# Kernel optimization log

Hardware: AMD Instinct MI355X
Metric: run time of the kernel (lower is better)

Reference implementation:

```python
import jax, jax.numpy as jnp
import numpy as np

N = 100000   # nodes
E = 3200000  # edges
G = 512      # graphs in batch
EPS = 1e-5   # batchnorm eps


def _lin(key, fan_in, fan_out):
    return jax.random.normal(key, (fan_in, fan_out), jnp.float32) / np.sqrt(fan_in)


def setup_inputs() -> dict:
    key = jax.random.key(0)
    ks = jax.random.split(key, 12)
    x = jax.random.normal(ks[0], (N, 2), jnp.float32)
    edge_index = jax.random.randint(ks[1], (2, E), 0, N, dtype=jnp.int64)
    batch_index = jnp.sort(jax.random.randint(ks[2], (N,), 0, G, dtype=jnp.int64))
    w = (8, 32, 128)
    return {
        "x": x, "edge_index": edge_index, "batch_index": batch_index,
        "W1": _lin(ks[3], 2, w[0]),   "b1": jnp.zeros((w[0],), jnp.float32),
        "g1": jnp.ones((w[0],), jnp.float32),  "be1": jnp.zeros((w[0],), jnp.float32),
        "W2": _lin(ks[4], w[0], w[1]), "b2": jnp.zeros((w[1],), jnp.float32),
        "g2": jnp.ones((w[1],), jnp.float32),  "be2": jnp.zeros((w[1],), jnp.float32),
        "W3": _lin(ks[5], w[1], w[2]), "b3": jnp.zeros((w[2],), jnp.float32),
        "g3": jnp.ones((w[2],), jnp.float32),  "be3": jnp.zeros((w[2],), jnp.float32),
        "Wl": _lin(ks[6], w[2], 3),    "bl": jnp.zeros((3,), jnp.float32),
    }


def _gcn_norm(edge_index):
    # add self loops, symmetric normalization (PyG GCNConv default)
    loops = jnp.arange(N, dtype=edge_index.dtype)
    src = jnp.concatenate([edge_index[0], loops])
    dst = jnp.concatenate([edge_index[1], loops])
    deg = jax.ops.segment_sum(jnp.ones_like(dst, jnp.float32), dst, num_segments=N)
    dis = jnp.where(deg > 0, jax.lax.rsqrt(jnp.maximum(deg, 1.0)), 0.0)
    norm = dis[src] * dis[dst]  # [E+N]
    return src, dst, norm


def _gcn_conv(h, W, b, src, dst, norm):
    h = h @ W                                   # [N, out]
    msg = h[src] * norm[:, None]                # gather + scale
    return jax.ops.segment_sum(msg, dst, num_segments=N) + b


def _bn(h, g, b):
    # training-mode batchnorm over node dim
    m = jnp.mean(h, axis=0)
    v = jnp.mean(jnp.square(h - m), axis=0)
    return (h - m) * jax.lax.rsqrt(v + EPS) * g + b


def reference(x, edge_index, batch_index, W1, b1, g1, be1, W2, b2, g2, be2,
              W3, b3, g3, be3, Wl, bl):
    src, dst, norm = _gcn_norm(edge_index)
    h = _bn(jax.nn.relu(_gcn_conv(x, W1, b1, src, dst, norm)), g1, be1)
    h = _bn(jax.nn.relu(_gcn_conv(h, W2, b2, src, dst, norm)), g2, be2)
    h = _bn(jax.nn.relu(_gcn_conv(h, W3, b3, src, dst, norm)), g3, be3)
    pooled = jax.ops.segment_max(h, batch_index, num_segments=G)  # [G, 128]
    logits = pooled @ Wl + bl                                     # [G, 3]
    return jax.nn.log_softmax(logits, axis=1)
```

## Files before the change

### kernel.cpp

```cpp
#include <hip/hip_runtime.h>
#include <hip/hip_bf16.h>
#include <hip/hip_fp16.h>
#include <math.h>

#define N_NODES 100000
#define N_EDGES 3200000
#define N_GRAPHS 512
#define BN_EPS 1e-5f
#define NBIN ((N_NODES + 511) / 512)
#define CHUNK 8192
#define NCHUNK ((N_EDGES + CHUNK - 1) / CHUNK)
#define STORE_CAP (N_EDGES + 16 * NBIN * NCHUNK)
#define NMMB ((N_NODES + 63) / 64)
#define NB2 3125
#define NB2P 3136
#define PLANE2 ((size_t)(N_NODES + 1) * 16)
#define PLANEU ((size_t)N_NODES * 16)
#define A1CAP 1024
#define A2CAP 2048
#define A3CAP 2048

typedef _Float16 half8_t __attribute__((ext_vector_type(8)));
typedef float float4_t __attribute__((ext_vector_type(4)));

struct alignas(8) h4 { __half2 a, b; };
struct alignas(16) h8s { __half2 h[4]; };



__global__ void k_hist2(const int* __restrict__ dst, int* __restrict__ hists) {
    __shared__ int h[NBIN];
    for (int i = threadIdx.x; i < NBIN; i += blockDim.x) h[i] = 0;
    __syncthreads();
    int e0 = blockIdx.x * CHUNK;
    int e1 = min(e0 + CHUNK, N_EDGES);
    int e = e0 + threadIdx.x * 8;
    if (e + 8 <= e1) {
        int4 d0 = *(const int4*)(dst + e);
        int4 d1 = *(const int4*)(dst + e + 4);
        atomicAdd(&h[d0.x >> 9], 1); atomicAdd(&h[d0.y >> 9], 1);
        atomicAdd(&h[d0.z >> 9], 1); atomicAdd(&h[d0.w >> 9], 1);
        atomicAdd(&h[d1.x >> 9], 1); atomicAdd(&h[d1.y >> 9], 1);
        atomicAdd(&h[d1.z >> 9], 1); atomicAdd(&h[d1.w >> 9], 1);
    } else {
        for (; e < e1; ++e) atomicAdd(&h[dst[e] >> 9], 1);
    }
    __syncthreads();
    for (int i = threadIdx.x; i < NBIN; i += blockDim.x)
        hists[i * NCHUNK + blockIdx.x] = h[i];
}

__global__ void k_scan2(int* __restrict__ hists, int* __restrict__ ghist) {
    int b = blockIdx.x;
    int lane = threadIdx.x;
    int carry = 0;
    int base = b * NCHUNK;
    for (int c0 = 0; c0 < NCHUNK; c0 += 64) {
        int c = c0 + lane;
        int v = (c < NCHUNK) ? hists[base + c] : 0;
        int pv = (v + 15) & ~15;
        int inc = pv;
#pragma unroll
        for (int off = 1; off < 64; off <<= 1) {
            int u = __shfl_up(inc, off, 64);
            if (lane >= off) inc += u;
        }
        if (c < NCHUNK) hists[base + c] = inc - pv + carry;
        carry += __shfl(inc, 63, 64);
    }
    if (lane == 0) ghist[b] = carry;
}

__global__ void k_binscan(const int* __restrict__ ghist, int* __restrict__ bbase) {
    __shared__ int sd[512];
    int t = threadIdx.x;
    int v = (t < NBIN) ? ghist[t] : 0;
    sd[t] = v;
    __syncthreads();
    for (int off = 1; off < 512; off <<= 1) {
        int u = (t >= off) ? sd[t - off] : 0;
        __syncthreads();
        sd[t] += u;
        __syncthreads();
    }
    if (t < NBIN) bbase[t] = sd[t] - v;
    if (t == 511) bbase[NBIN] = sd[511];
}

__global__ void k_scatter(const int* __restrict__ src, const int* __restrict__ dst,
                          const int* __restrict__ bbase, const int* __restrict__ hists,
                          int* __restrict__ store) {
    __shared__ int cur[NBIN];
    for (int i = threadIdx.x; i < NBIN; i += blockDim.x)
        cur[i] = bbase[i] + hists[i * NCHUNK + blockIdx.x];
    __syncthreads();
    int e0 = blockIdx.x * CHUNK;
    int e1 = min(e0 + CHUNK, N_EDGES);
    int e = e0 + threadIdx.x * 8;
    if (e + 8 <= e1) {
        int4 d0 = *(const int4*)(dst + e), d1 = *(const int4*)(dst + e + 4);
        int4 s0 = *(const int4*)(src + e), s1 = *(const int4*)(src + e + 4);
        int dd[8] = {d0.x, d0.y, d0.z, d0.w, d1.x, d1.y, d1.z, d1.w};
        int sv[8] = {s0.x, s0.y, s0.z, s0.w, s1.x, s1.y, s1.z, s1.w};
#pragma unroll
        for (int j = 0; j < 8; ++j) {
            int d = dd[j];
            int b = d >> 9;
            int pos = atomicAdd(&cur[b], 1);
            store[pos] = (sv[j] << 9) | (d & 511);
        }
    } else {
        for (; e < e1; ++e) {
            int d = dst[e];
            int b = d >> 9;
            int pos = atomicAdd(&cur[b], 1);
            store[pos] = (src[e] << 9) | (d & 511);
        }
    }
    __syncthreads();
    for (int i = threadIdx.x; i < NBIN; i += blockDim.x) {
        int p = cur[i];
        int end = (p + 15) & ~15;
        for (; p < end; ++p) store[p] = -1;
    }
}

__global__ void k_csr_build(const int* __restrict__ bbase, const int* __restrict__ store,
                            const float* __restrict__ x, int* __restrict__ offs,
                            int* __restrict__ ends, float* __restrict__ dis,
                            float* __restrict__ rdis, float4* __restrict__ xd,
                            int* __restrict__ csr) {
    __shared__ int cnt[512], cur[512], wsum[4];
    int b = blockIdx.x;
    int n0 = b << 9;
    int e0 = bbase[b], e1 = bbase[b + 1];
    int t = threadIdx.x;
    int lane = t & 63, wid = t >> 6;
    if (t < 512) cnt[t] = 0;
    __syncthreads();
    for (int e = e0 + t; e < e1; e += 4096) {
        int p[4];
#pragma unroll
        for (int j = 0; j < 4; ++j)
            p[j] = (e + 1024 * j < e1) ? store[e + 1024 * j] : -1;
#pragma unroll
        for (int j = 0; j < 4; ++j)
            if (p[j] >= 0) atomicAdd(&cnt[p[j] & 511], 1);
    }
    __syncthreads();
    int c0 = 0, c1 = 0, pair = 0, inc = 0;
    if (t < 256) {
        c0 = cnt[2 * t];
        c1 = cnt[2 * t + 1];
        pair = c0 + c1;
        inc = pair;
#pragma unroll
        for (int off = 1; off < 64; off <<= 1) {
            int u = __shfl_up(inc, off, 64);
            if (lane >= off) inc += u;
        }
        if (lane == 63) wsum[wid] = inc;
    }
    __syncthreads();
    if (t < 256) {
        int wo = 0;
        for (int w = 0; w < wid; ++w) wo += wsum[w];
        int ex = inc - pair + wo;
        cur[2 * t] = ex;
        cur[2 * t + 1] = ex + c0;
#pragma unroll
        for (int j = 0; j < 2; ++j) {
            int n = n0 + 2 * t + j;
            int cc = j ? c1 : c0;
            int exx = j ? ex + c0 : ex;
            if (n < N_NODES) {
                offs[n] = e0 + exx;
                ends[n] = e0 + exx + cc;
                float dn = rsqrtf(1.0f + (float)cc);
                dis[n] = dn;
                rdis[n] = sqrtf(1.0f + (float)cc);
                float2 xv = *(const float2*)(x + 2 * (size_t)n);
                xd[n] = make_float4(dn * xv.x, dn * xv.y, dn, 0.f);
            } else if (n == N_NODES) {
                xd[N_NODES] = make_float4(0.f, 0.f, 0.f, 0.f);
            }
        }
    }
    __syncthreads();
    for (int e = e0 + t; e < e1; e += 4096) {
        int p[4];
#pragma unroll
        for (int j = 0; j < 4; ++j)
            p[j] = (e + 1024 * j < e1) ? store[e + 1024 * j] : -1;
#pragma unroll
        for (int j = 0; j < 4; ++j)
            if (p[j] >= 0) {
                int pos = e0 + atomicAdd(&cur[p[j] & 511], 1);
                csr[pos] = p[j] >> 9;
            }
    }
}


__global__ void k_agg1(const float4* __restrict__ xd, const int* __restrict__ offs,
                       const int* __restrict__ ends, const int* __restrict__ csr,
                       const float* __restrict__ W1, const float* __restrict__ b1,
                       float* __restrict__ svec, __half* __restrict__ ys1) {
    __shared__ float sW[16], sb[8];
    __shared__ int sidx[A1CAP], soff[16], send[16];
    int t = threadIdx.x;
    int n0 = blockIdx.x * 16;
    if (t < 16) { sW[t] = W1[t]; soff[t] = offs[n0 + t]; send[t] = ends[n0 + t]; }
    if (t >= 16 && t < 24) sb[t - 16] = b1[t - 16];
    __syncthreads();
    int base = soff[0];
    int span = send[15] - base;
    int cap = min(span, A1CAP);
    for (int i = t; i < cap; i += 256) sidx[i] = csr[base + i];
    __syncthreads();

    int nl = t >> 4;
    int lane16 = t & 15;
    int node = n0 + nl;
    int rb = soff[nl] - base;
    int re = send[nl] - base;
    float ax = 0.f, ay = 0.f, as = 0.f;
    for (int r = rb + lane16; r < re; r += 64) {
        int s[4];
#pragma unroll
        for (int j = 0; j < 4; ++j) {
            int rr = r + 16 * j;
            s[j] = (rr < re) ? ((rr < A1CAP) ? sidx[rr] : csr[base + rr]) : N_NODES;
        }
        float4 v[4];
#pragma unroll
        for (int j = 0; j < 4; ++j) v[j] = xd[s[j]];
#pragma unroll
        for (int j = 0; j < 4; ++j) {
            ax += v[j].x;
            ay += v[j].y;
            as += v[j].z;
        }
    }
#pragma unroll
    for (int off = 1; off < 16; off <<= 1) {
        ax += __shfl_xor(ax, off, 64);
        ay += __shfl_xor(ay, off, 64);
        as += __shfl_xor(as, off, 64);
    }
    if (lane16 == 0) {
        float4 xn = xd[node];
        float dn = xn.z;
        float u0x = dn * (ax + xn.x);
        float u0y = dn * (ay + xn.y);
        svec[node] = dn * (as + xn.z);
        float y[8];
#pragma unroll
        for (int f = 0; f < 8; ++f)
            y[f] = dn * fmaxf(u0x * sW[f] + u0y * sW[8 + f] + sb[f], 0.f);
        h8s o;
#pragma unroll
        for (int q = 0; q < 4; ++q) o.h[q] = __floats2half2_rn(y[2 * q], y[2 * q + 1]);
        *(h8s*)(ys1 + (size_t)node * 8) = o;
    }
}


__global__ void k_stats8v(const __half* __restrict__ ys1, const float* __restrict__ rdis,
                          float* __restrict__ stats) {
    int t = threadIdx.x;
    float s[8] = {0, 0, 0, 0, 0, 0, 0, 0};
    float s2[8] = {0, 0, 0, 0, 0, 0, 0, 0};
    for (int n = blockIdx.x * 256 + t; n < N_NODES; n += gridDim.x * 256) {
        float r = rdis[n];
        h8s v = *(const h8s*)(ys1 + (size_t)n * 8);
#pragma unroll
        for (int q = 0; q < 4; ++q) {
            float v0 = __low2float(v.h[q]) * r;
            float v1 = __high2float(v.h[q]) * r;
            s[2 * q] += v0;      s2[2 * q] += v0 * v0;
            s[2 * q + 1] += v1;  s2[2 * q + 1] += v1 * v1;
        }
    }
#pragma unroll
    for (int off = 1; off < 64; off <<= 1)
#pragma unroll
        for (int k = 0; k < 8; ++k) {
            s[k] += __shfl_xor(s[k], off, 64);
            s2[k] += __shfl_xor(s2[k], off, 64);
        }
    __shared__ float sm[16];
    if (t < 16) sm[t] = 0.f;
    __syncthreads();
    if ((t & 63) == 0) {
#pragma unroll
        for (int k = 0; k < 8; ++k) {
            atomicAdd(&sm[k], s[k]);
            atomicAdd(&sm[8 + k], s2[k]);
        }
    }
    __syncthreads();
    if (t < 16) atomicAdd(&stats[t], sm[t]);
}


__global__ void k_prep2(const float* __restrict__ stats, const float* __restrict__ gamma,
                        const float* __restrict__ beta, const float* __restrict__ W2,
                        float* __restrict__ W2p, float* __restrict__ cw2,
                        __half* __restrict__ ys1) {
    __shared__ float a1[8], c1[8];
    int t = threadIdx.x;
    if (t < 8) {
        float inv_n = 1.0f / (float)N_NODES;
        float m = stats[t] * inv_n;
        float v = stats[8 + t] * inv_n - m * m;
        float a = gamma[t] * rsqrtf(v + BN_EPS);
        a1[t] = a;
        c1[t] = beta[t] - m * a;
    }
    __syncthreads();
    W2p[t] = a1[t >> 5] * W2[t];
    if (t < 32) {
        float cb = 0.f;
#pragma unroll
        for (int i = 0; i < 8; ++i) cb += c1[i] * W2[i * 32 + t];
        cw2[t] = cb;
    }
    if (t == 128) *(int4*)(ys1 + (size_t)N_NODES * 8) = make_int4(0, 0, 0, 0);
}


__global__ void k_agg2(const __half* __restrict__ ys1, const int* __restrict__ offs,
                       const int* __restrict__ ends, const int* __restrict__ csr,
                       const float* __restrict__ dis, const float* __restrict__ svec,
                       const float* __restrict__ W2p, const float* __restrict__ cw2,
                       const float* __restrict__ b2, __half* __restrict__ ys2,
                       float* __restrict__ part2) {
    __shared__ float sW[256], sC[32], sB[32], sm2[64];
    __shared__ int sidx[A2CAP], soff[32], send[32];
    int t = threadIdx.x;
    int n0 = blockIdx.x * 32;
    sW[t] = W2p[t];
    if (t < 32) {
        sC[t] = cw2[t]; sB[t] = b2[t];
        soff[t] = offs[n0 + t]; send[t] = ends[n0 + t];
    }
    if (t < 64) sm2[t] = 0.f;
    __syncthreads();
    int base = soff[0];
    int span = send[31] - base;
    int cap = min(span, A2CAP);
    for (int i = t; i < cap; i += 256) sidx[i] = csr[base + i];
    __syncthreads();

    int nl = t >> 3;
    int lane8 = t & 7;
    int node = n0 + nl;
    int rb = soff[nl] - base;
    int re = send[nl] - base;
    float a[8] = {0, 0, 0, 0, 0, 0, 0, 0};
    int r = rb + lane8;
    if (span <= A2CAP) {
        for (; r + 24 < re; r += 32) {
            int s0 = sidx[r], s1 = sidx[r + 8], s2i = sidx[r + 16], s3 = sidx[r + 24];
            h8s v0 = *(const h8s*)(ys1 + (size_t)s0 * 8);
            h8s v1 = *(const h8s*)(ys1 + (size_t)s1 * 8);
            h8s v2 = *(const h8s*)(ys1 + (size_t)s2i * 8);
            h8s v3 = *(const h8s*)(ys1 + (size_t)s3 * 8);
#pragma unroll
            for (int q = 0; q < 4; ++q) {
                a[2 * q] += __low2float(v0.h[q]) + __low2float(v1.h[q]) +
                            __low2float(v2.h[q]) + __low2float(v3.h[q]);
                a[2 * q + 1] += __high2float(v0.h[q]) + __high2float(v1.h[q]) +
                                __high2float(v2.h[q]) + __high2float(v3.h[q]);
            }
        }
        if (r < re) {
            int s[4];
#pragma unroll
            for (int j = 0; j < 4; ++j) {
                int rr = r + 8 * j;
                s[j] = (rr < re) ? sidx[rr] : N_NODES;
            }
            h8s v[4];
#pragma unroll
            for (int j = 0; j < 4; ++j) v[j] = *(const h8s*)(ys1 + (size_t)s[j] * 8);
#pragma unroll
            for (int j = 0; j < 4; ++j)
#pragma unroll
                for (int q = 0; q < 4; ++q) {
                    a[2 * q] += __low2float(v[j].h[q]);
                    a[2 * q + 1] += __high2float(v[j].h[q]);
                }
        }
    } else {
        for (; r < re; r += 32) {
            int s[4];
#pragma unroll
            for (int j = 0; j < 4; ++j) {
                int rr = r + 8 * j;
                s[j] = (rr < re) ? ((rr < A2CAP) ? sidx[rr] : csr[base + rr]) : N_NODES;
            }
            h8s v[4];
#pragma unroll
            for (int j = 0; j < 4; ++j) v[j] = *(const h8s*)(ys1 + (size_t)s[j] * 8);
#pragma unroll
            for (int j = 0; j < 4; ++j)
#pragma unroll
                for (int q = 0; q < 4; ++q) {
                    a[2 * q] += __low2float(v[j].h[q]);
                    a[2 * q + 1] += __high2float(v[j].h[q]);
                }
        }
    }
    if (lane8 == 0) {
        h8s v = *(const h8s*)(ys1 + (size_t)node * 8);
#pragma unroll
        for (int q = 0; q < 4; ++q) {
            a[2 * q] += __low2float(v.h[q]);
            a[2 * q + 1] += __high2float(v.h[q]);
        }
    }
#pragma unroll
    for (int off = 1; off < 8; off <<= 1)
#pragma unroll
        for (int k = 0; k < 8; ++k) a[k] += __shfl_xor(a[k], off, 64);
    int lane = t & 63;
    int nsub = lane >> 3;
    int lb = nsub << 3;
    float u[8];
#pragma unroll
    for (int i = 0; i < 8; ++i) u[i] = __shfl(a[i], lb, 64);
    float dn = dis[node];
    float sv = svec[node];
#pragma unroll
    for (int i = 0; i < 8; ++i) u[i] *= dn;
    int c0 = (lane & 7) * 4;
    float hh[4], hs2[4];
#pragma unroll
    for (int k = 0; k < 4; ++k) {
        int col = c0 + k;
        float conv = sB[col] + sv * sC[col];
#pragma unroll
        for (int i = 0; i < 8; ++i) conv += u[i] * sW[i * 32 + col];
        hh[k] = fmaxf(conv, 0.f);
        hs2[k] = hh[k] * hh[k];
    }
    h4 o;
    o.a = __floats2half2_rn(dn * hh[0], dn * hh[1]);
    o.b = __floats2half2_rn(dn * hh[2], dn * hh[3]);
    *(h4*)(ys2 + (size_t)(c0 >> 4) * PLANE2 + (size_t)node * 16 + (c0 & 15)) = o;

    float hs[4];
#pragma unroll
    for (int k = 0; k < 4; ++k) hs[k] = hh[k];
#pragma unroll
    for (int off = 8; off < 64; off <<= 1)
#pragma unroll
        for (int k = 0; k < 4; ++k) {
            hs[k] += __shfl_xor(hs[k], off, 64);
            hs2[k] += __shfl_xor(hs2[k], off, 64);
        }
    if (nsub == 0) {
#pragma unroll
        for (int k = 0; k < 4; ++k) {
            atomicAdd(&sm2[c0 + k], hs[k]);
            atomicAdd(&sm2[32 + c0 + k], hs2[k]);
        }
    }
    __syncthreads();
    if (t < 64) part2[(size_t)t * NB2P + blockIdx.x] = sm2[t];
}

__global__ void k_red32(const float* __restrict__ part2, float* __restrict__ stats2) {
    int i = blockIdx.x;
    int t = threadIdx.x;
    float s = 0.f;
    for (int b = t; b < NB2; b += 256) s += part2[(size_t)i * NB2P + b];
    __shared__ float sm[256];
    sm[t] = s;
    __syncthreads();
    for (int st = 128; st > 0; st >>= 1) {
        if (t < st) sm[t] += sm[t + st];
        __syncthreads();
    }
    if (t == 0) stats2[i] = sm[0];
}


__global__ void k_prep3(const float* __restrict__ stats, const float* __restrict__ gamma,
                        const float* __restrict__ beta, const float* __restrict__ W3,
                        __half* __restrict__ wfrag, float* __restrict__ cw3,
                        __half* __restrict__ ys2) {
    __shared__ float a2[32], c2[32];
    int t = threadIdx.x;
    if (t < 32) {
        float inv_n = 1.0f / (float)N_NODES;
        float m = stats[t] * inv_n;
        float v = stats[32 + t] * inv_n - m * m;
        float a = gamma[t] * rsqrtf(v + BN_EPS);
        a2[t] = a;
        c2[t] = beta[t] - m * a;
    }
    __syncthreads();
    {
        int g = t >> 6, kq = (t >> 4) & 3, c = t & 15;
#pragma unroll
        for (int j = 0; j < 8; ++j) {
            int k = kq * 8 + j;
            wfrag[(size_t)t * 8 + j] = __float2half(a2[k] * W3[k * 128 + g * 16 + c]);
        }
    }
    if (t < 128) {
        float cb = 0.f;
#pragma unroll
        for (int k = 0; k < 32; ++k) cb += c2[k] * W3[k * 128 + t];
        cw3[t] = cb;
    }
    if (t >= 480 && t < 496) {
        int idx = t - 480;
        ((__half2*)(ys2 + (size_t)(idx >> 3) * PLANE2 + (size_t)N_NODES * 16))[idx & 7] =
            __half2{__float2half(0.f), __float2half(0.f)};
    }
}


__global__ void k_agg3(const __half* __restrict__ ys2, const int* __restrict__ offs,
                       const int* __restrict__ ends, const int* __restrict__ csr,
                       const float* __restrict__ dis, __half* __restrict__ u2) {
    __shared__ int sidx[A3CAP], soff[32], send[32];
    int plane = blockIdx.x & 1;
    int nb = blockIdx.x >> 1;
    int t = threadIdx.x;
    int n0 = nb * 32;
    if (t < 32) { soff[t] = offs[n0 + t]; send[t] = ends[n0 + t]; }
    __syncthreads();
    int base = soff[0];
    int span = send[31] - base;
    int cap = min(span, A3CAP);
    for (int i = t; i < cap; i += 512) sidx[i] = csr[base + i];
    __syncthreads();

    int nl = t >> 4;
    int lane16 = t & 15;
    int eg = lane16 >> 1;
    int chunk = lane16 & 1;
    int node = n0 + nl;
    int rb = soff[nl] - base;
    int re = send[nl] - base;
    float a[8] = {0, 0, 0, 0, 0, 0, 0, 0};
    const __half* hp = ys2 + (size_t)plane * PLANE2 + chunk * 8;
    int r = rb + eg;
    if (span <= A3CAP) {
        for (; r + 24 < re; r += 32) {
            int s0 = sidx[r], s1 = sidx[r + 8], s2i = sidx[r + 16], s3 = sidx[r + 24];
            h8s v0 = *(const h8s*)(hp + (size_t)s0 * 16);
            h8s v1 = *(const h8s*)(hp + (size_t)s1 * 16);
            h8s v2 = *(const h8s*)(hp + (size_t)s2i * 16);
            h8s v3 = *(const h8s*)(hp + (size_t)s3 * 16);
#pragma unroll
            for (int q = 0; q < 4; ++q) {
                a[2 * q] += __low2float(v0.h[q]) + __low2float(v1.h[q]) +
                            __low2float(v2.h[q]) + __low2float(v3.h[q]);
                a[2 * q + 1] += __high2float(v0.h[q]) + __high2float(v1.h[q]) +
                                __high2float(v2.h[q]) + __high2float(v3.h[q]);
            }
        }
        if (r < re) {
            int s[4];
#pragma unroll
            for (int j = 0; j < 4; ++j) {
                int rr = r + 8 * j;
                s[j] = (rr < re) ? sidx[rr] : N_NODES;
            }
            h8s v[4];
#pragma unroll
            for (int j = 0; j < 4; ++j) v[j] = *(const h8s*)(hp + (size_t)s[j] * 16);
#pragma unroll
            for (int j = 0; j < 4; ++j)
#pragma unroll
                for (int q = 0; q < 4; ++q) {
                    a[2 * q] += __low2float(v[j].h[q]);
                    a[2 * q + 1] += __high2float(v[j].h[q]);
                }
        }
    } else {
        for (; r < re; r += 32) {
            int s[4];
#pragma unroll
            for (int j = 0; j < 4; ++j) {
                int rr = r + 8 * j;
                s[j] = (rr < re) ? ((rr < A3CAP) ? sidx[rr] : csr[base + rr]) : N_NODES;
            }
            h8s v[4];
#pragma unroll
            for (int j = 0; j < 4; ++j) v[j] = *(const h8s*)(hp + (size_t)s[j] * 16);
#pragma unroll
            for (int j = 0; j < 4; ++j)
#pragma unroll
                for (int q = 0; q < 4; ++q) {
                    a[2 * q] += __low2float(v[j].h[q]);
                    a[2 * q + 1] += __high2float(v[j].h[q]);
                }
        }
    }
    if (eg == 0) {
        h8s v = *(const h8s*)(hp + (size_t)node * 16);
#pragma unroll
        for (int q = 0; q < 4; ++q) {
            a[2 * q] += __low2float(v.h[q]);
            a[2 * q + 1] += __high2float(v.h[q]);
        }
    }
#pragma unroll
    for (int off = 2; off < 16; off <<= 1)
#pragma unroll
        for (int k = 0; k < 8; ++k) a[k] += __shfl_xor(a[k], off, 64);
    if (eg == 0) {
        float dn = dis[node];
        h8s o;
#pragma unroll
        for (int q = 0; q < 4; ++q)
            o.h[q] = __floats2half2_rn(dn * a[2 * q], dn * a[2 * q + 1]);
        *(h8s*)(u2 + (size_t)plane * PLANEU + (size_t)node * 16 + chunk * 8) = o;
    }
}


__global__ void k_mm_mfma(const __half* __restrict__ u2, const __half* __restrict__ wfrag,
                          const float* __restrict__ cw3, const float* __restrict__ b3,
                          const float* __restrict__ svec, const int* __restrict__ batch,
                          float* __restrict__ spart, int* __restrict__ gmax,
                          int* __restrict__ gmin) {
    __shared__ float sm[256];
    int t = threadIdx.x;
    int wave = t >> 6;
    int lane = t & 63;
    int n0 = (blockIdx.x * 4 + wave) * 16;
    bool active = n0 < N_NODES;
    int m = lane & 15;
    int kq = lane >> 4;
    float ss[8] = {0, 0, 0, 0, 0, 0, 0, 0};
    float ss2[8] = {0, 0, 0, 0, 0, 0, 0, 0};

    if (active) {
        half8_t af = *(const half8_t*)(u2 + (size_t)(kq >> 1) * PLANEU +
                                       (size_t)(n0 + m) * 16 + (kq & 1) * 8);
        float4_t accs[8];
#pragma unroll
        for (int g = 0; g < 8; ++g) {
            float4_t acc = {0.f, 0.f, 0.f, 0.f};
            half8_t bf = *(const half8_t*)(wfrag + (size_t)((g * 4 + kq) * 16 + m) * 8);
            accs[g] = __builtin_amdgcn_mfma_f32_16x16x32_f16(af, bf, acc, 0, 0, 0);
        }
        float sv[4];
#pragma unroll
        for (int r = 0; r < 4; ++r) sv[r] = svec[n0 + kq * 4 + r];

        int b_first = batch[n0];
        int b_last = batch[n0 + 15];
        bool uni = (b_first == b_last);
        int bnr[4];
        if (!uni) {
#pragma unroll
            for (int r = 0; r < 4; ++r) bnr[r] = batch[n0 + kq * 4 + r];
        }
        float ymx[8], ymn[8];
#pragma unroll
        for (int g = 0; g < 8; ++g) {
            float cwf = cw3[g * 16 + m];
            float bf3 = b3[g * 16 + m];
            float mx = 0.f, mn = INFINITY;
#pragma unroll
            for (int r = 0; r < 4; ++r) {
                float y = fmaxf(accs[g][r] + sv[r] * cwf + bf3, 0.f);
                ss[g] += y;
                ss2[g] += y * y;
                mx = fmaxf(mx, y);
                mn = fminf(mn, y);
                if (!uni) {
                    int yb = __float_as_int(y);
                    atomicMax(&gmax[bnr[r] * 128 + g * 16 + m], yb);
                    atomicMin(&gmin[bnr[r] * 128 + g * 16 + m], yb);
                }
            }
            ymx[g] = mx;
            ymn[g] = mn;
        }
        if (uni) {
#pragma unroll
            for (int off = 16; off < 64; off <<= 1)
#pragma unroll
                for (int g = 0; g < 8; ++g) {
                    ymx[g] = fmaxf(ymx[g], __shfl_xor(ymx[g], off, 64));
                    ymn[g] = fminf(ymn[g], __shfl_xor(ymn[g], off, 64));
                }
            if (kq == 0) {
#pragma unroll
                for (int g = 0; g < 8; ++g) {
                    atomicMax(&gmax[b_first * 128 + g * 16 + m], __float_as_int(ymx[g]));
                    atomicMin(&gmin[b_first * 128 + g * 16 + m], __float_as_int(ymn[g]));
                }
            }
        }
    }
#pragma unroll
    for (int off = 16; off < 64; off <<= 1)
#pragma unroll
        for (int g = 0; g < 8; ++g) {
            ss[g] += __shfl_xor(ss[g], off, 64);
            ss2[g] += __shfl_xor(ss2[g], off, 64);
        }
    sm[t] = 0.f;
    __syncthreads();
    if (active && kq == 0) {
#pragma unroll
        for (int g = 0; g < 8; ++g) {
            atomicAdd(&sm[g * 16 + m], ss[g]);
            atomicAdd(&sm[128 + g * 16 + m], ss2[g]);
        }
    }
    __syncthreads();
    spart[(size_t)blockIdx.x * 256 + t] = sm[t];
}

__global__ void k_stats_red(const float* __restrict__ part, float* __restrict__ stats) {
    int i = blockIdx.x;
    int t = threadIdx.x;
    float s = 0.f;
    for (int b = t; b < NMMB; b += 256) s += part[(size_t)b * 256 + i];
    __shared__ float sm[256];
    sm[t] = s;
    __syncthreads();
    for (int st = 128; st > 0; st >>= 1) {
        if (t < st) sm[t] += sm[t + st];
        __syncthreads();
    }
    if (t == 0) stats[i] = sm[0];
}


__device__ __forceinline__ int lower_bound_dev(const int* __restrict__ a, int val) {
    int lo = 0, hi = N_NODES;
    while (lo < hi) {
        int mid = (lo + hi) >> 1;
        if (a[mid] < val) lo = mid + 1; else hi = mid;
    }
    return lo;
}

__global__ void k_poolhead(const int* __restrict__ gmax, const int* __restrict__ gmin,
                           const int* __restrict__ batch, const float* __restrict__ stats,
                           const float* __restrict__ gamma, const float* __restrict__ beta,
                           const float* __restrict__ Wl, const float* __restrict__ bl,
                           float* __restrict__ out) {
    int g = blockIdx.x;
    int f = threadIdx.x;
    float inv_n = 1.0f / (float)N_NODES;
    float m = stats[f] * inv_n;
    float var = stats[128 + f] * inv_n - m * m;
    float a = gamma[f] * rsqrtf(var + BN_EPS);
    float c = beta[f] - m * a;
    int s = lower_bound_dev(batch, g);
    int e = lower_bound_dev(batch, g + 1);
    float mx = __int_as_float(gmax[g * 128 + f]);
    float mn = __int_as_float(gmin[g * 128 + f]);
    float r;
    if (e > s) r = (a >= 0.f) ? (a * mx + c) : (a * mn + c);
    else r = -INFINITY;
    __shared__ float l[3][128];
    l[0][f] = r * Wl[f * 3 + 0];
    l[1][f] = r * Wl[f * 3 + 1];
    l[2][f] = r * Wl[f * 3 + 2];
    __syncthreads();
    for (int st = 64; st > 0; st >>= 1) {
        if (f < st) {
            l[0][f] += l[0][f + st];
            l[1][f] += l[1][f + st];
            l[2][f] += l[2][f + st];
        }
        __syncthreads();
    }
    if (f == 0) {
        float l0 = l[0][0] + bl[0], l1 = l[1][0] + bl[1], l2 = l[2][0] + bl[2];
        float mxl = fmaxf(l0, fmaxf(l1, l2));
        float lse = mxl + logf(expf(l0 - mxl) + expf(l1 - mxl) + expf(l2 - mxl));
        out[g * 3 + 0] = l0 - lse;
        out[g * 3 + 1] = l1 - lse;
        out[g * 3 + 2] = l2 - lse;
    }
}


extern "C" void kernel_launch(void* const* d_in, const int* in_sizes, int n_in,
                              void* d_out, int out_size, void* d_ws, size_t ws_size,
                              hipStream_t stream) {
    const float* x   = (const float*)d_in[0];
    const int* ei    = (const int*)d_in[1];
    const int* src   = ei;
    const int* dst   = ei + N_EDGES;
    const int* batch = (const int*)d_in[2];
    const float *W1 = (const float*)d_in[3],  *b1 = (const float*)d_in[4];
    const float *g1 = (const float*)d_in[5],  *be1 = (const float*)d_in[6];
    const float *W2 = (const float*)d_in[7],  *b2 = (const float*)d_in[8];
    const float *g2 = (const float*)d_in[9],  *be2 = (const float*)d_in[10];
    const float *W3 = (const float*)d_in[11], *b3 = (const float*)d_in[12];
    const float *g3 = (const float*)d_in[13], *be3 = (const float*)d_in[14];
    const float *Wl = (const float*)d_in[15], *bl = (const float*)d_in[16];
    float* out = (float*)d_out;

    int* base = (int*)d_ws;
    size_t o = 0;
    float* stats1 = (float*)(base + o); o += 256;
    float* stats2 = (float*)(base + o); o += 256;
    float* stats3 = (float*)(base + o); o += 256;
    int* gmax     = base + o; o += (size_t)N_GRAPHS * 128;
    size_t zero_words = o;
    int* gmin     = base + o; o += (size_t)N_GRAPHS * 128;
    int* bbase    = base + o; o += NBIN + 4;
    int* ghist    = base + o; o += NBIN + 4;
    int* hists    = base + o; o += ((size_t)NBIN * NCHUNK + 3) & ~3ULL;
    float* W2p    = (float*)(base + o); o += 256;
    float* cw2    = (float*)(base + o); o += 32;
    __half* wfrag = (__half*)(base + o); o += 2048;
    float* cw3    = (float*)(base + o); o += 128;
    int* offs     = base + o; o += 100000;
    int* ends     = base + o; o += 100000;
    int* store    = base + o; o += STORE_CAP;
    int* csr      = base + o; o += STORE_CAP;
    float* dis    = (float*)(base + o); o += N_NODES;
    float* rdis   = (float*)(base + o); o += N_NODES;
    float* svec   = (float*)(base + o); o += N_NODES;
    float* spart  = (float*)(base + o); o += (size_t)NMMB * 256;
    float* part2  = (float*)(base + o); o += (size_t)64 * NB2P;
    float4* xd    = (float4*)(base + o); o += (size_t)(N_NODES + 1) * 4;
    __half* ys1   = (__half*)(base + o); o += (size_t)(N_NODES + 1) * 4;
    __half* ys2   = (__half*)(base + o); o += (size_t)(N_NODES + 1) * 16;
    __half* u2    = (__half*)(base + o); o += (size_t)N_NODES * 16;
    if (ws_size < o * 4) return;

    const int TB = 256;

    hipMemsetAsync(base, 0, zero_words * 4, stream);
    hipMemsetAsync(gmin, 0x7F, (size_t)N_GRAPHS * 128 * 4, stream);

    k_hist2<<<NCHUNK, 1024, 0, stream>>>(dst, hists);
    k_scan2<<<NBIN, 64, 0, stream>>>(hists, ghist);
    k_binscan<<<1, 512, 0, stream>>>(ghist, bbase);
    k_scatter<<<NCHUNK, 1024, 0, stream>>>(src, dst, bbase, hists, store);
    k_csr_build<<<NBIN, 1024, 0, stream>>>(bbase, store, x, offs, ends, dis, rdis, xd, csr);

    k_agg1<<<N_NODES / 16, TB, 0, stream>>>(xd, offs, ends, csr, W1, b1, svec, ys1);
    k_stats8v<<<64, 256, 0, stream>>>(ys1, rdis, stats1);
    k_prep2<<<1, 256, 0, stream>>>(stats1, g1, be1, W2, W2p, cw2, ys1);

    k_agg2<<<NB2, TB, 0, stream>>>(ys1, offs, ends, csr, dis, svec, W2p, cw2, b2, ys2, part2);
    k_red32<<<64, 256, 0, stream>>>(part2, stats2);
    k_prep3<<<1, 512, 0, stream>>>(stats2, g2, be2, W3, wfrag, cw3, ys2);

    k_agg3<<<2 * (N_NODES / 32), 512, 0, stream>>>(ys2, offs, ends, csr, dis, u2);
    k_mm_mfma<<<NMMB, 256, 0, stream>>>(u2, wfrag, cw3, b3, svec, batch, spart, gmax, gmin);
    k_stats_red<<<256, 256, 0, stream>>>(spart, stats3);

    k_poolhead<<<N_GRAPHS, 128, 0, stream>>>(gmax, gmin, batch, stats3, g3, be3, Wl, bl, out);
}
```

Measured before the change: 313.4 us.

## Interleave layer-2 features into contiguous 32-wide rows, single-pass layer-3 aggregation

```diff
diff --git a/kernel.cpp b/kernel.cpp
--- a/kernel.cpp
+++ b/kernel.cpp
@@ -14,8 +14,6 @@
 #define NMMB ((N_NODES + 63) / 64)
 #define NB2 3125
 #define NB2P 3136
-#define PLANE2 ((size_t)(N_NODES + 1) * 16)
-#define PLANEU ((size_t)N_NODES * 16)
 #define A1CAP 1024
 #define A2CAP 2048
 #define A3CAP 2048
@@ -449,7 +447,7 @@
     h4 o;
     o.a = __floats2half2_rn(dn * hh[0], dn * hh[1]);
     o.b = __floats2half2_rn(dn * hh[2], dn * hh[3]);
-    *(h4*)(ys2 + (size_t)(c0 >> 4) * PLANE2 + (size_t)node * 16 + (c0 & 15)) = o;
+    *(h4*)(ys2 + (size_t)node * 32 + c0) = o;
 
     float hs[4];
 #pragma unroll
@@ -519,7 +517,7 @@
     }
     if (t >= 480 && t < 496) {
         int idx = t - 480;
-        ((__half2*)(ys2 + (size_t)(idx >> 3) * PLANE2 + (size_t)N_NODES * 16))[idx & 7] =
+        ((__half2*)(ys2 + (size_t)N_NODES * 32))[idx] =
             __half2{__float2half(0.f), __float2half(0.f)};
     }
 }
@@ -529,10 +527,8 @@
                        const int* __restrict__ ends, const int* __restrict__ csr,
                        const float* __restrict__ dis, __half* __restrict__ u2) {
     __shared__ int sidx[A3CAP], soff[32], send[32];
-    int plane = blockIdx.x & 1;
-    int nb = blockIdx.x >> 1;
-    int t = threadIdx.x;
-    int n0 = nb * 32;
+    int t = threadIdx.x;
+    int n0 = blockIdx.x * 32;
     if (t < 32) { soff[t] = offs[n0 + t]; send[t] = ends[n0 + t]; }
     __syncthreads();
     int base = soff[0];
@@ -548,22 +544,32 @@
     int node = n0 + nl;
     int rb = soff[nl] - base;
     int re = send[nl] - base;
-    float a[8] = {0, 0, 0, 0, 0, 0, 0, 0};
-    const __half* hp = ys2 + (size_t)plane * PLANE2 + chunk * 8;
+    float a[16];
+#pragma unroll
+    for (int k = 0; k < 16; ++k) a[k] = 0.f;
+    const __half* hp = ys2 + chunk * 16;
     int r = rb + eg;
     if (span <= A3CAP) {
         for (; r + 24 < re; r += 32) {
             int s0 = sidx[r], s1 = sidx[r + 8], s2i = sidx[r + 16], s3 = sidx[r + 24];
-            h8s v0 = *(const h8s*)(hp + (size_t)s0 * 16);
-            h8s v1 = *(const h8s*)(hp + (size_t)s1 * 16);
-            h8s v2 = *(const h8s*)(hp + (size_t)s2i * 16);
-            h8s v3 = *(const h8s*)(hp + (size_t)s3 * 16);
+            h8s v0a = *(const h8s*)(hp + (size_t)s0 * 32);
+            h8s v0b = *(const h8s*)(hp + (size_t)s0 * 32 + 8);
+            h8s v1a = *(const h8s*)(hp + (size_t)s1 * 32);
+            h8s v1b = *(const h8s*)(hp + (size_t)s1 * 32 + 8);
+            h8s v2a = *(const h8s*)(hp + (size_t)s2i * 32);
+            h8s v2b = *(const h8s*)(hp + (size_t)s2i * 32 + 8);
+            h8s v3a = *(const h8s*)(hp + (size_t)s3 * 32);
+            h8s v3b = *(const h8s*)(hp + (size_t)s3 * 32 + 8);
 #pragma unroll
             for (int q = 0; q < 4; ++q) {
-                a[2 * q] += __low2float(v0.h[q]) + __low2float(v1.h[q]) +
-                            __low2float(v2.h[q]) + __low2float(v3.h[q]);
-                a[2 * q + 1] += __high2float(v0.h[q]) + __high2float(v1.h[q]) +
-                                __high2float(v2.h[q]) + __high2float(v3.h[q]);
+                a[2 * q] += __low2float(v0a.h[q]) + __low2float(v1a.h[q]) +
+                            __low2float(v2a.h[q]) + __low2float(v3a.h[q]);
+                a[2 * q + 1] += __high2float(v0a.h[q]) + __high2float(v1a.h[q]) +
+                                __high2float(v2a.h[q]) + __high2float(v3a.h[q]);
+                a[8 + 2 * q] += __low2float(v0b.h[q]) + __low2float(v1b.h[q]) +
+                                __low2float(v2b.h[q]) + __low2float(v3b.h[q]);
+                a[8 + 2 * q + 1] += __high2float(v0b.h[q]) + __high2float(v1b.h[q]) +
+                                    __high2float(v2b.h[q]) + __high2float(v3b.h[q]);
             }
         }
         if (r < re) {
@@ -573,16 +579,18 @@
                 int rr = r + 8 * j;
                 s[j] = (rr < re) ? sidx[rr] : N_NODES;
             }
-            h8s v[4];
-#pragma unroll
-            for (int j = 0; j < 4; ++j) v[j] = *(const h8s*)(hp + (size_t)s[j] * 16);
-#pragma unroll
-            for (int j = 0; j < 4; ++j)
+#pragma unroll
+            for (int j = 0; j < 4; ++j) {
+                h8s va = *(const h8s*)(hp + (size_t)s[j] * 32);
+                h8s vb = *(const h8s*)(hp + (size_t)s[j] * 32 + 8);
 #pragma unroll
                 for (int q = 0; q < 4; ++q) {
-                    a[2 * q] += __low2float(v[j].h[q]);
-                    a[2 * q + 1] += __high2float(v[j].h[q]);
+                    a[2 * q] += __low2float(va.h[q]);
+                    a[2 * q + 1] += __high2float(va.h[q]);
+                    a[8 + 2 * q] += __low2float(vb.h[q]);
+                    a[8 + 2 * q + 1] += __high2float(vb.h[q]);
                 }
+            }
         }
     } else {
         for (; r < re; r += 32) {
@@ -592,37 +600,45 @@
                 int rr = r + 8 * j;
                 s[j] = (rr < re) ? ((rr < A3CAP) ? sidx[rr] : csr[base + rr]) : N_NODES;
             }
-            h8s v[4];
-#pragma unroll
-            for (int j = 0; j < 4; ++j) v[j] = *(const h8s*)(hp + (size_t)s[j] * 16);
-#pragma unroll
-            for (int j = 0; j < 4; ++j)
+#pragma unroll
+            for (int j = 0; j < 4; ++j) {
+                h8s va = *(const h8s*)(hp + (size_t)s[j] * 32);
+                h8s vb = *(const h8s*)(hp + (size_t)s[j] * 32 + 8);
 #pragma unroll
                 for (int q = 0; q < 4; ++q) {
-                    a[2 * q] += __low2float(v[j].h[q]);
-                    a[2 * q + 1] += __high2float(v[j].h[q]);
+                    a[2 * q] += __low2float(va.h[q]);
+                    a[2 * q + 1] += __high2float(va.h[q]);
+                    a[8 + 2 * q] += __low2float(vb.h[q]);
+                    a[8 + 2 * q + 1] += __high2float(vb.h[q]);
                 }
+            }
         }
     }
     if (eg == 0) {
-        h8s v = *(const h8s*)(hp + (size_t)node * 16);
+        h8s va = *(const h8s*)(hp + (size_t)node * 32);
+        h8s vb = *(const h8s*)(hp + (size_t)node * 32 + 8);
 #pragma unroll
         for (int q = 0; q < 4; ++q) {
-            a[2 * q] += __low2float(v.h[q]);
-            a[2 * q + 1] += __high2float(v.h[q]);
+            a[2 * q] += __low2float(va.h[q]);
+            a[2 * q + 1] += __high2float(va.h[q]);
+            a[8 + 2 * q] += __low2float(vb.h[q]);
+            a[8 + 2 * q + 1] += __high2float(vb.h[q]);
         }
     }
 #pragma unroll
     for (int off = 2; off < 16; off <<= 1)
 #pragma unroll
-        for (int k = 0; k < 8; ++k) a[k] += __shfl_xor(a[k], off, 64);
+        for (int k = 0; k < 16; ++k) a[k] += __shfl_xor(a[k], off, 64);
     if (eg == 0) {
         float dn = dis[node];
-        h8s o;
-#pragma unroll
-        for (int q = 0; q < 4; ++q)
-            o.h[q] = __floats2half2_rn(dn * a[2 * q], dn * a[2 * q + 1]);
-        *(h8s*)(u2 + (size_t)plane * PLANEU + (size_t)node * 16 + chunk * 8) = o;
+        h8s oa, ob;
+#pragma unroll
+        for (int q = 0; q < 4; ++q) {
+            oa.h[q] = __floats2half2_rn(dn * a[2 * q], dn * a[2 * q + 1]);
+            ob.h[q] = __floats2half2_rn(dn * a[8 + 2 * q], dn * a[8 + 2 * q + 1]);
+        }
+        *(h8s*)(u2 + (size_t)node * 32 + chunk * 16) = oa;
+        *(h8s*)(u2 + (size_t)node * 32 + chunk * 16 + 8) = ob;
     }
 }
 
@@ -644,8 +660,7 @@
     float ss2[8] = {0, 0, 0, 0, 0, 0, 0, 0};
 
     if (active) {
-        half8_t af = *(const half8_t*)(u2 + (size_t)(kq >> 1) * PLANEU +
-                                       (size_t)(n0 + m) * 16 + (kq & 1) * 8);
+        half8_t af = *(const half8_t*)(u2 + (size_t)(n0 + m) * 32 + kq * 8);
         float4_t accs[8];
 #pragma unroll
         for (int g = 0; g < 8; ++g) {
@@ -858,7 +873,7 @@
     k_red32<<<64, 256, 0, stream>>>(part2, stats2);
     k_prep3<<<1, 512, 0, stream>>>(stats2, g2, be2, W3, wfrag, cw3, ys2);
 
-    k_agg3<<<2 * (N_NODES / 32), 512, 0, stream>>>(ys2, offs, ends, csr, dis, u2);
+    k_agg3<<<N_NODES / 32, 512, 0, stream>>>(ys2, offs, ends, csr, dis, u2);
     k_mm_mfma<<<NMMB, 256, 0, stream>>>(u2, wfrag, cw3, b3, svec, batch, spart, gmax, gmin);
     k_stats_red<<<256, 256, 0, stream>>>(spart, stats3);
 
```

After: 323.2 us. 1.03x slower.
